# Optimization experiments

Hardware: AMD Instinct MI355X
Metric: run time of the kernel (lower is better)

The kernel has to match this reference:

```python
import jax, jax.numpy as jnp
import numpy as np
from jax import lax

EMBED = 64


def setup_inputs() -> dict:
    key = jax.random.key(0)
    ks = jax.random.split(key, 5)
    b, l, v, e, h = 256, 1024, 96, 64, 256
    x = jax.random.randint(ks[0], (b, l), 0, v, dtype=jnp.int64)
    hidden = jnp.zeros((b, h), dtype=jnp.float32)
    # xavier-uniform-like init (scale by fan sums)
    emb = jax.random.normal(ks[1], (v, e), dtype=jnp.float32) * 0.1
    W_ih = jax.random.normal(ks[2], (e + h, h), dtype=jnp.float32) * (1.0 / np.sqrt(e + h))
    b_ih = jnp.zeros((h,), dtype=jnp.float32)
    W_ho = jax.random.normal(ks[3], (h, v), dtype=jnp.float32) * (1.0 / np.sqrt(h))
    b_ho = jnp.zeros((v,), dtype=jnp.float32)
    return {"x": x, "hidden": hidden, "emb": emb, "W_ih": W_ih, "b_ih": b_ih,
            "W_ho": W_ho, "b_ho": b_ho}


def reference(x, hidden, emb, W_ih, b_ih, W_ho, b_ho):
    # x: [b, l] int indices; hidden: [b, h]
    x_embed = emb[x]                      # [b, l, e]
    Wx, Wh = W_ih[:EMBED], W_ih[EMBED:]   # split cat([x, h]) @ W_ih
    # precompute input projections for all timesteps (batched GEMM)
    xproj = jnp.einsum('ble,eh->blh', x_embed, Wx) + b_ih  # [b, l, h]

    def step(h_prev, xp_t):
        h_t = jnp.tanh(xp_t + h_prev @ Wh)  # [b, h]
        return h_t, h_t

    final_hidden, hs = lax.scan(step, hidden, xproj.transpose(1, 0, 2))  # hs: [l, b, h]
    hs = hs.transpose(1, 0, 2)                     # [b, l, h]
    logits = jnp.einsum('blh,hv->blv', hs, W_ho) + b_ho  # [b, l, v]
    return logits, final_hidden
```

## Files before the change

### kernel.cpp

```cpp
#include <hip/hip_runtime.h>
#include <hip/hip_bf16.h>

#define Lv 1024
#define Vv 96
#define Ev 64
#define Hv 256
#define ROWS 16
#define HOFF (256 * 1024 * 96)
#define EPAD 72
#define HB 4096
#define TSL 65536

typedef __attribute__((ext_vector_type(8))) short bf16x8;
typedef __attribute__((ext_vector_type(4))) float f32x4;
typedef __attribute__((ext_vector_type(2))) unsigned int u32x2;

__device__ __forceinline__ unsigned short f2b(float f) {
  unsigned u = __builtin_bit_cast(unsigned, f);
  return (unsigned short)((u + 0x7fffu + ((u >> 16) & 1u)) >> 16);
}
__device__ __forceinline__ unsigned cvtpk_bf16(float lo, float hi) {
  unsigned r;
  asm("v_cvt_pk_bf16_f32 %0, %1, %2" : "=v"(r) : "v"(lo), "v"(hi));
  return r;
}
__device__ __forceinline__ float fast_tanh(float x) {
  float e = __builtin_amdgcn_exp2f(x * 2.885390081777927f);
  return 1.0f - 2.0f * __builtin_amdgcn_rcpf(e + 1.0f);
}
__device__ __forceinline__ void step_barrier() {
  asm volatile("s_waitcnt lgkmcnt(0)\n\ts_barrier" ::: "memory");
  __builtin_amdgcn_sched_barrier(0);
}

__global__ void detect_i64(const int* __restrict__ x, int* __restrict__ flag) {
  if (threadIdx.x == 0 && blockIdx.x == 0) {
    int ok = 1;
    for (int i = 0; i < 64; ++i) ok &= (x[2 * i + 1] == 0);
    *flag = ok;
  }
}

__global__ __launch_bounds__(512, 2) void rnn8t(
    const int* __restrict__ x, const float* __restrict__ h0,
    const float* __restrict__ emb, const float* __restrict__ W_ih,
    const float* __restrict__ b_ih, float* __restrict__ out,
    unsigned short* __restrict__ hs, const int* __restrict__ flagp) {
  const int tid = threadIdx.x;
  const int w = tid >> 6, ln = tid & 63, lm = ln & 15, g = ln >> 4;
  const int r0 = blockIdx.x * ROWS;

  __shared__ __attribute__((aligned(16))) unsigned short s_h[2 * HB];
  __shared__ __attribute__((aligned(16))) unsigned short s_emb[Vv * EPAD];
  __shared__ unsigned char s_x[Lv * ROWS];

  const int flag = *flagp;

  for (int idx = tid; idx < Vv * Ev; idx += 512)
    s_emb[(idx >> 6) * EPAD + (idx & 63)] = f2b(emb[idx]);
  for (int idx = tid; idx < ROWS * Hv; idx += 512) {
    int b_ = idx >> 8, hd = idx & 255;
    s_h[HB + b_ * 256 + ((((hd >> 3) ^ (b_ & 7)) << 3) | (hd & 7))] =
        f2b(h0[(r0 + b_) * Hv + hd]);
  }
  for (int idx = tid; idx < ROWS * Lv; idx += 512) {
    int t = idx >> 4, row = idx & 15;
    long long src = (long long)(r0 + row) * Lv + t;
    int v = flag ? x[2 * src] : x[src];
    s_x[t * ROWS + row] = (unsigned char)v;
  }

  bf16x8 wh[2][8], wx[2][2];
  f32x4 bihv[2];
#pragma unroll
  for (int nt = 0; nt < 2; ++nt) {
    const int n = 32 * w + 16 * nt + lm;
#pragma unroll
    for (int kf = 0; kf < 8; ++kf)
#pragma unroll
      for (int i = 0; i < 8; ++i)
        wh[nt][kf][i] = (short)f2b(W_ih[(Ev + 32 * kf + 8 * g + i) * Hv + n]);
#pragma unroll
    for (int kf = 0; kf < 2; ++kf)
#pragma unroll
      for (int i = 0; i < 8; ++i)
        wx[nt][kf][i] = (short)f2b(W_ih[(32 * kf + 8 * g + i) * Hv + n]);
    bihv[nt] = *(const f32x4*)&b_ih[32 * w + 16 * nt + 4 * g];
  }

  const unsigned short* ra[8];
#pragma unroll
  for (int kf = 0; kf < 8; ++kf)
    ra[kf] = &s_h[lm * 256 + (((4 * kf + g) ^ (lm & 7)) << 3)];
  unsigned short* wa[2];
#pragma unroll
  for (int nt = 0; nt < 2; ++nt)
    wa[nt] = &s_h[lm * 256 + (((4 * w + 2 * nt + (g >> 1)) ^ (lm & 7)) << 3) +
                  ((g & 1) << 2)];
  unsigned short* hp = hs + (size_t)(r0 + lm) * 256 + 32 * w + 4 * g;

  __syncthreads();

  bf16x8 ef0, ef1;
  int xi_n;
  {
    int xi0 = s_x[lm];
    const unsigned short* ep = &s_emb[xi0 * EPAD + 8 * g];
    ef0 = *(const bf16x8*)ep;
    ef1 = *(const bf16x8*)(ep + 32);
    xi_n = s_x[ROWS + lm];
  }

#define STEPB(TT, RB, WB, LAST)                                                   \
  do {                                                                            \
    bf16x8 af[8];                                                                 \
    _Pragma("unroll") for (int kf = 0; kf < 8; ++kf)                              \
        af[kf] = *(const bf16x8*)(ra[kf] + (RB));                                 \
                           \
    f32x4 a0 = bihv[0];                                                           \
    a0 = __builtin_amdgcn_mfma_f32_16x16x32_bf16(wx[0][0], ef0, a0, 0, 0, 0);     \
    a0 = __builtin_amdgcn_mfma_f32_16x16x32_bf16(wx[0][1], ef1, a0, 0, 0, 0);     \
    _Pragma("unroll") for (int kf = 0; kf < 8; ++kf)                              \
        a0 = __builtin_amdgcn_mfma_f32_16x16x32_bf16(wh[0][kf], af[kf], a0, 0, 0, 0); \
    float h0v = fast_tanh(a0[0]), h1v = fast_tanh(a0[1]);                         \
    float h2v = fast_tanh(a0[2]), h3v = fast_tanh(a0[3]);                         \
    u32x2 p0;                                                                     \
    p0[0] = cvtpk_bf16(h0v, h1v);                                                 \
    p0[1] = cvtpk_bf16(h2v, h3v);                                                 \
    *(u32x2*)(wa[0] + (WB)) = p0;                  \
    *(u32x2*)hp = p0;                                           \
                                                        \
    f32x4 a1 = bihv[1];                                                           \
    a1 = __builtin_amdgcn_mfma_f32_16x16x32_bf16(wx[1][0], ef0, a1, 0, 0, 0);     \
    a1 = __builtin_amdgcn_mfma_f32_16x16x32_bf16(wx[1][1], ef1, a1, 0, 0, 0);     \
    _Pragma("unroll") for (int kf = 0; kf < 8; ++kf)                              \
        a1 = __builtin_amdgcn_mfma_f32_16x16x32_bf16(wh[1][kf], af[kf], a1, 0, 0, 0); \
    {                        \
      const unsigned short* ep = &s_emb[xi_n * EPAD + 8 * g];                     \
      ef0 = *(const bf16x8*)ep;                                                   \
      ef1 = *(const bf16x8*)(ep + 32);                                            \
      int tn = ((TT) + 2 < Lv) ? (TT) + 2 : (Lv - 1);                             \
      xi_n = s_x[tn * ROWS + lm];                                                 \
    }                                                                             \
    float h4v = fast_tanh(a1[0]), h5v = fast_tanh(a1[1]);                         \
    float h6v = fast_tanh(a1[2]), h7v = fast_tanh(a1[3]);                         \
    u32x2 p1;                                                                     \
    p1[0] = cvtpk_bf16(h4v, h5v);                                                 \
    p1[1] = cvtpk_bf16(h6v, h7v);                                                 \
    *(u32x2*)(wa[1] + (WB)) = p1;                                                 \
    *(u32x2*)(hp + 16) = p1;                                    \
    hp += TSL;                                                                    \
    if (LAST) {                                                                   \
      float* fo = out + HOFF + (size_t)(r0 + lm) * Hv + 32 * w + 4 * g;           \
      *(f32x4*)fo = (f32x4){h0v, h1v, h2v, h3v};                                  \
      *(f32x4*)(fo + 16) = (f32x4){h4v, h5v, h6v, h7v};                           \
    }                                                                             \
    step_barrier();                                                               \
  } while (0)

  STEPB(0, HB, 0, 0);
  for (int t = 1; t < Lv - 1; t += 2) {
    STEPB(t, 0, HB, 0);
    STEPB(t + 1, HB, 0, 0);
  }
  STEPB(Lv - 1, 0, HB, 1);
#undef STEPB
}

__global__ __launch_bounds__(512, 2) void logits_gemm(
    const unsigned short* __restrict__ hs, const float* __restrict__ W_ho,
    const float* __restrict__ b_ho, float* __restrict__ out) {
  const int tid = threadIdx.x;
  const int w = tid >> 6, ln = tid & 63, lm = ln & 15, g = ln >> 4;
  const int tg = blockIdx.x >> 2, bg = blockIdx.x & 3;

  __shared__ __attribute__((aligned(16))) unsigned short s_who[3072 * 8];
  for (int f = tid; f < 3072; f += 512) {
    int vt = f >> 9, kf = (f >> 6) & 7, lane = f & 63;
    int k0 = 32 * kf + 8 * (lane >> 4), v = 16 * vt + (lane & 15);
    bf16x8 fr;
#pragma unroll
    for (int i = 0; i < 8; ++i) fr[i] = (short)f2b(W_ho[(k0 + i) * Vv + v]);
    *(bf16x8*)&s_who[f * 8] = fr;
  }
  __syncthreads();

  const int bt = w & 3, vg = w >> 2;
  const int b0 = bg * 64 + bt * 16;
  const int j0 = vg * 3;
  float bb[3];
#pragma unroll
  for (int jj = 0; jj < 3; ++jj) bb[jj] = b_ho[16 * (j0 + jj) + lm];

#pragma unroll
  for (int tt = 0; tt < 4; ++tt) {
    const int t = tg * 4 + tt;
    const unsigned short* hpb = hs + (size_t)t * TSL + (b0 + lm) * 256 + 8 * g;
    f32x4 acc[3];
#pragma unroll
    for (int jj = 0; jj < 3; ++jj)
      acc[jj] = (f32x4){bb[jj], bb[jj], bb[jj], bb[jj]};
#pragma unroll
    for (int kf = 0; kf < 8; ++kf) {
      bf16x8 af = *(const bf16x8*)(hpb + 32 * kf);
#pragma unroll
      for (int jj = 0; jj < 3; ++jj) {
        bf16x8 bw = *(const bf16x8*)&s_who[(((j0 + jj) * 8 + kf) * 64 + ln) * 8];
        acc[jj] =
            __builtin_amdgcn_mfma_f32_16x16x32_bf16(af, bw, acc[jj], 0, 0, 0);
      }
    }
#pragma unroll
    for (int jj = 0; jj < 3; ++jj)
#pragma unroll
      for (int rr = 0; rr < 4; ++rr)
        out[(size_t)(b0 + 4 * g + rr) * (Lv * Vv) + (size_t)t * Vv +
            16 * (j0 + jj) + lm] = acc[jj][rr];
  }
}

__global__ __launch_bounds__(512, 2) void rnn8(
    const int* __restrict__ x, const float* __restrict__ h0,
    const float* __restrict__ emb, const float* __restrict__ W_ih,
    const float* __restrict__ b_ih, const float* __restrict__ W_ho,
    const float* __restrict__ b_ho, float* __restrict__ out,
    const int* __restrict__ flagp) {
  const int tid = threadIdx.x;
  const int w = tid >> 6, ln = tid & 63, lm = ln & 15, g = ln >> 4;
  const int r0 = blockIdx.x * ROWS;

  __shared__ __attribute__((aligned(16))) unsigned short s_emb[Vv * EPAD];
  __shared__ __attribute__((aligned(16))) unsigned short s_h[2 * HB];
  __shared__ unsigned char s_x[Lv * ROWS];

  const int flag = *flagp;

  for (int idx = tid; idx < Vv * Ev; idx += 512)
    s_emb[(idx >> 6) * EPAD + (idx & 63)] = f2b(emb[idx]);
  for (int idx = tid; idx < ROWS * Hv; idx += 512) {
    int m = idx >> 8, nn = idx & 255;
    s_h[HB + (m << 8) + ((((nn >> 3) ^ (m & 7)) << 3) | (nn & 7))] =
        f2b(h0[(r0 + m) * Hv + nn]);
  }
  for (int idx = tid; idx < ROWS * Lv; idx += 512) {
    int row = idx >> 10, t = idx & 1023;
    long long src = (long long)(r0 + row) * Lv + t;
    int v = flag ? x[2 * src] : x[src];
    s_x[t * ROWS + row] = (unsigned char)v;
  }

  bf16x8 wh[2][8], wx[2][2], who[8];
  float bih[2], bhov = 0.0f;
#pragma unroll
  for (int nt = 0; nt < 2; ++nt) {
    const int n = 32 * w + 16 * nt + lm;
    bih[nt] = b_ih[n];
#pragma unroll
    for (int kf = 0; kf < 8; ++kf)
#pragma unroll
      for (int i = 0; i < 8; ++i)
        wh[nt][kf][i] = (short)f2b(W_ih[(Ev + 32 * kf + 8 * g + i) * Hv + n]);
#pragma unroll
    for (int kf = 0; kf < 2; ++kf)
#pragma unroll
      for (int i = 0; i < 8; ++i)
        wx[nt][kf][i] = (short)f2b(W_ih[(32 * kf + 8 * g + i) * Hv + n]);
  }
  if (w < 6) {
    const int n = 16 * w + lm;
    bhov = b_ho[n];
#pragma unroll
    for (int kf = 0; kf < 8; ++kf)
#pragma unroll
      for (int i = 0; i < 8; ++i)
        who[kf][i] = (short)f2b(W_ho[(32 * kf + 8 * g + i) * Vv + n]);
  }

  const unsigned short* ra[8];
#pragma unroll
  for (int kf = 0; kf < 8; ++kf)
    ra[kf] = &s_h[(lm << 8) + (((4 * kf + g) ^ (lm & 7)) << 3)];
  unsigned short* wa[8];
#pragma unroll
  for (int nt = 0; nt < 2; ++nt)
#pragma unroll
    for (int rr = 0; rr < 4; ++rr) {
      int m = 4 * g + rr, n = 32 * w + 16 * nt + lm;
      wa[nt * 4 + rr] = &s_h[(m << 8) + ((((n >> 3) ^ (m & 7)) << 3) | (n & 7))];
    }
  float* ob[4] = {out, out, out, out};
  if (w < 6) {
#pragma unroll
    for (int rr = 0; rr < 4; ++rr)
      ob[rr] = out + (size_t)(r0 + 4 * g + rr) * (Lv * Vv) + 16 * w + lm;
  }

  __syncthreads();

  bf16x8 ef0, ef1;
  {
    int xi = s_x[lm];
    const unsigned short* ep = &s_emb[xi * EPAD + 8 * g];
    ef0 = *(const bf16x8*)ep;
    ef1 = *(const bf16x8*)(ep + 32);
  }

#define STEP8(TT, RB, WB, DOLOG, LAST)                                             \
  do {                                                                             \
    bf16x8 af[8];                                                                  \
    _Pragma("unroll") for (int kf = 0; kf < 8; ++kf)                               \
        af[kf] = *(const bf16x8*)(ra[kf] + (RB));                                  \
    f32x4 a0 = {bih[0], bih[0], bih[0], bih[0]};                                   \
    f32x4 a1 = {bih[1], bih[1], bih[1], bih[1]};                                   \
    a0 = __builtin_amdgcn_mfma_f32_16x16x32_bf16(ef0, wx[0][0], a0, 0, 0, 0);      \
    a1 = __builtin_amdgcn_mfma_f32_16x16x32_bf16(ef0, wx[1][0], a1, 0, 0, 0);      \
    a0 = __builtin_amdgcn_mfma_f32_16x16x32_bf16(ef1, wx[0][1], a0, 0, 0, 0);      \
    a1 = __builtin_amdgcn_mfma_f32_16x16x32_bf16(ef1, wx[1][1], a1, 0, 0, 0);      \
    _Pragma("unroll") for (int kf = 0; kf < 8; ++kf) {                             \
      a0 = __builtin_amdgcn_mfma_f32_16x16x32_bf16(af[kf], wh[0][kf], a0, 0, 0, 0);\
      a1 = __builtin_amdgcn_mfma_f32_16x16x32_bf16(af[kf], wh[1][kf], a1, 0, 0, 0);\
    }                                                                              \
    if ((DOLOG) && w < 6) {                                                        \
      f32x4 l = {bhov, bhov, bhov, bhov};                                          \
      _Pragma("unroll") for (int kf = 0; kf < 8; ++kf)                             \
          l = __builtin_amdgcn_mfma_f32_16x16x32_bf16(af[kf], who[kf], l, 0, 0, 0);\
      const size_t o = (size_t)((TT)-1) * Vv;                                      \
      ob[0][o] = l[0]; ob[1][o] = l[1]; ob[2][o] = l[2]; ob[3][o] = l[3];          \
    }                                                                              \
    {                                                                              \
      int tn = ((TT) + 1 < Lv) ? (TT) + 1 : (Lv - 1);                              \
      int xi = s_x[tn * ROWS + lm];                                                \
      const unsigned short* ep = &s_emb[xi * EPAD + 8 * g];                        \
      ef0 = *(const bf16x8*)ep;                                                    \
      ef1 = *(const bf16x8*)(ep + 32);                                             \
    }                                                                              \
    float th0 = fast_tanh(a0[0]), th1 = fast_tanh(a0[1]);                          \
    float th2 = fast_tanh(a0[2]), th3 = fast_tanh(a0[3]);                          \
    float th4 = fast_tanh(a1[0]), th5 = fast_tanh(a1[1]);                          \
    float th6 = fast_tanh(a1[2]), th7 = fast_tanh(a1[3]);                          \
    unsigned p01 = cvtpk_bf16(th0, th1), p23 = cvtpk_bf16(th2, th3);               \
    unsigned p45 = cvtpk_bf16(th4, th5), p67 = cvtpk_bf16(th6, th7);               \
    wa[0][WB] = (unsigned short)p01;                                               \
    wa[1][WB] = (unsigned short)(p01 >> 16);                                       \
    wa[2][WB] = (unsigned short)p23;                                               \
    wa[3][WB] = (unsigned short)(p23 >> 16);                                       \
    wa[4][WB] = (unsigned short)p45;                                               \
    wa[5][WB] = (unsigned short)(p45 >> 16);                                       \
    wa[6][WB] = (unsigned short)p67;                                               \
    wa[7][WB] = (unsigned short)(p67 >> 16);                                       \
    if (LAST) {                                                                    \
      float* fh = out + HOFF + (size_t)(r0 + 4 * g) * Hv + 32 * w + lm;            \
      fh[0 * Hv] = th0; fh[1 * Hv] = th1; fh[2 * Hv] = th2; fh[3 * Hv] = th3;      \
      fh[0 * Hv + 16] = th4; fh[1 * Hv + 16] = th5;                                \
      fh[2 * Hv + 16] = th6; fh[3 * Hv + 16] = th7;                                \
    }                                                                              \
    asm volatile("s_waitcnt lgkmcnt(0)\n\ts_barrier" ::: "memory");                \
    __builtin_amdgcn_sched_barrier(0);                                             \
  } while (0)

  STEP8(0, HB, 0, 0, 0);
  for (int t = 1; t < Lv - 1; t += 2) {
    STEP8(t, 0, HB, 1, 0);
    STEP8(t + 1, HB, 0, 1, 0);
  }
  STEP8(Lv - 1, 0, HB, 1, 1);

  if (w < 6) {
    bf16x8 af[8];
#pragma unroll
    for (int kf = 0; kf < 8; ++kf) af[kf] = *(const bf16x8*)(ra[kf] + HB);
    f32x4 l = {bhov, bhov, bhov, bhov};
#pragma unroll
    for (int kf = 0; kf < 8; ++kf)
      l = __builtin_amdgcn_mfma_f32_16x16x32_bf16(af[kf], who[kf], l, 0, 0, 0);
    const size_t o = (size_t)(Lv - 1) * Vv;
    ob[0][o] = l[0]; ob[1][o] = l[1]; ob[2][o] = l[2]; ob[3][o] = l[3];
  }
#undef STEP8
}

extern "C" void kernel_launch(void* const* d_in, const int* in_sizes, int n_in,
                              void* d_out, int out_size, void* d_ws, size_t ws_size,
                              hipStream_t stream) {
  const int* x     = (const int*)d_in[0];
  const float* h0  = (const float*)d_in[1];
  const float* emb = (const float*)d_in[2];
  const float* Wih = (const float*)d_in[3];
  const float* bih = (const float*)d_in[4];
  const float* Who = (const float*)d_in[5];
  const float* bho = (const float*)d_in[6];
  float* out = (float*)d_out;
  int* flag = (int*)d_ws;

  const size_t hs_bytes = (size_t)Lv * 256 * 256 * 2;
  detect_i64<<<1, 64, 0, stream>>>(x, flag);
  if (ws_size >= hs_bytes + 256) {
    unsigned short* hs = (unsigned short*)((char*)d_ws + 256);
    rnn8t<<<16, 512, 0, stream>>>(x, h0, emb, Wih, bih, out, hs, flag);
    logits_gemm<<<1024, 512, 0, stream>>>(hs, Who, bho, out);
  } else {
    rnn8<<<16, 512, 0, stream>>>(x, h0, emb, Wih, bih, Who, bho, out, flag);
  }
}
```

Measured before the change: 652.4 us.

## Split RNN batch across twice as many workgroups with eight rows each

The recurrent kernel now gives each workgroup 8 batch rows instead of 16 and launches 32 workgroups instead of 16, so more compute units work on the sequential recurrence at the same time. The MFMA tiles are still 16 wide, so lanes 8-15 duplicate rows 0-7 and only the lower half writes results. This shortens per-step work per CU only through more parallel blocks, not fewer MFMAs per block. Half of the MFMA work in each block is wasted, and the per-step barrier and latency chain stay the same.

```diff
diff --git a/kernel.cpp b/kernel.cpp
--- a/kernel.cpp
+++ b/kernel.cpp
@@ -6,9 +6,11 @@
 #define Ev 64
 #define Hv 256
 #define ROWS 16
+#define NBP 8
 #define HOFF (256 * 1024 * 96)
 #define EPAD 72
 #define HB 4096
+#define HBP 2048
 #define TSL 65536
 
 typedef __attribute__((ext_vector_type(8))) short bf16x8;
@@ -41,33 +43,34 @@
   }
 }
 
-__global__ __launch_bounds__(512, 2) void rnn8t(
+__global__ __launch_bounds__(512, 2) void rnn8b(
     const int* __restrict__ x, const float* __restrict__ h0,
     const float* __restrict__ emb, const float* __restrict__ W_ih,
     const float* __restrict__ b_ih, float* __restrict__ out,
     unsigned short* __restrict__ hs, const int* __restrict__ flagp) {
   const int tid = threadIdx.x;
   const int w = tid >> 6, ln = tid & 63, lm = ln & 15, g = ln >> 4;
-  const int r0 = blockIdx.x * ROWS;
-
-  __shared__ __attribute__((aligned(16))) unsigned short s_h[2 * HB];
+  const int lmb = lm & (NBP - 1);
+  const int r0 = blockIdx.x * NBP;
+
+  __shared__ __attribute__((aligned(16))) unsigned short s_h[2 * HBP];
   __shared__ __attribute__((aligned(16))) unsigned short s_emb[Vv * EPAD];
-  __shared__ unsigned char s_x[Lv * ROWS];
+  __shared__ unsigned char s_x[Lv * NBP];
 
   const int flag = *flagp;
 
   for (int idx = tid; idx < Vv * Ev; idx += 512)
     s_emb[(idx >> 6) * EPAD + (idx & 63)] = f2b(emb[idx]);
-  for (int idx = tid; idx < ROWS * Hv; idx += 512) {
+  for (int idx = tid; idx < NBP * Hv; idx += 512) {
     int b_ = idx >> 8, hd = idx & 255;
-    s_h[HB + b_ * 256 + ((((hd >> 3) ^ (b_ & 7)) << 3) | (hd & 7))] =
+    s_h[HBP + b_ * 256 + ((((hd >> 3) ^ b_) << 3) | (hd & 7))] =
         f2b(h0[(r0 + b_) * Hv + hd]);
   }
-  for (int idx = tid; idx < ROWS * Lv; idx += 512) {
-    int t = idx >> 4, row = idx & 15;
+  for (int idx = tid; idx < NBP * Lv; idx += 512) {
+    int t = idx >> 3, row = idx & (NBP - 1);
     long long src = (long long)(r0 + row) * Lv + t;
     int v = flag ? x[2 * src] : x[src];
-    s_x[t * ROWS + row] = (unsigned char)v;
+    s_x[t * NBP + row] = (unsigned char)v;
   }
 
   bf16x8 wh[2][8], wx[2][2];
@@ -91,24 +94,24 @@
   const unsigned short* ra[8];
 #pragma unroll
   for (int kf = 0; kf < 8; ++kf)
-    ra[kf] = &s_h[lm * 256 + (((4 * kf + g) ^ (lm & 7)) << 3)];
+    ra[kf] = &s_h[lmb * 256 + (((4 * kf + g) ^ lmb) << 3)];
   unsigned short* wa[2];
 #pragma unroll
   for (int nt = 0; nt < 2; ++nt)
-    wa[nt] = &s_h[lm * 256 + (((4 * w + 2 * nt + (g >> 1)) ^ (lm & 7)) << 3) +
+    wa[nt] = &s_h[lmb * 256 + (((4 * w + 2 * nt + (g >> 1)) ^ lmb) << 3) +
                   ((g & 1) << 2)];
-  unsigned short* hp = hs + (size_t)(r0 + lm) * 256 + 32 * w + 4 * g;
+  unsigned short* hp = hs + (size_t)(r0 + lmb) * 256 + 32 * w + 4 * g;
 
   __syncthreads();
 
   bf16x8 ef0, ef1;
   int xi_n;
   {
-    int xi0 = s_x[lm];
+    int xi0 = s_x[lmb];
     const unsigned short* ep = &s_emb[xi0 * EPAD + 8 * g];
     ef0 = *(const bf16x8*)ep;
     ef1 = *(const bf16x8*)(ep + 32);
-    xi_n = s_x[ROWS + lm];
+    xi_n = s_x[NBP + lmb];
   }
 
 #define STEPB(TT, RB, WB, LAST)                                                   \
@@ -127,8 +130,10 @@
     u32x2 p0;                                                                     \
     p0[0] = cvtpk_bf16(h0v, h1v);                                                 \
     p0[1] = cvtpk_bf16(h2v, h3v);                                                 \
-    *(u32x2*)(wa[0] + (WB)) = p0;                  \
-    *(u32x2*)hp = p0;                                           \
+    if (lm < NBP) {                                                               \
+      *(u32x2*)(wa[0] + (WB)) = p0;                \
+      *(u32x2*)hp = p0;                                         \
+    }                                                                             \
                                                         \
     f32x4 a1 = bihv[1];                                                           \
     a1 = __builtin_amdgcn_mfma_f32_16x16x32_bf16(wx[1][0], ef0, a1, 0, 0, 0);     \
@@ -140,30 +145,32 @@
       ef0 = *(const bf16x8*)ep;                                                   \
       ef1 = *(const bf16x8*)(ep + 32);                                            \
       int tn = ((TT) + 2 < Lv) ? (TT) + 2 : (Lv - 1);                             \
-      xi_n = s_x[tn * ROWS + lm];                                                 \
+      xi_n = s_x[tn * NBP + lmb];                                                 \
     }                                                                             \
     float h4v = fast_tanh(a1[0]), h5v = fast_tanh(a1[1]);                         \
     float h6v = fast_tanh(a1[2]), h7v = fast_tanh(a1[3]);                         \
     u32x2 p1;                                                                     \
     p1[0] = cvtpk_bf16(h4v, h5v);                                                 \
     p1[1] = cvtpk_bf16(h6v, h7v);                                                 \
-    *(u32x2*)(wa[1] + (WB)) = p1;                                                 \
-    *(u32x2*)(hp + 16) = p1;                                    \
+    if (lm < NBP) {                                                               \
+      *(u32x2*)(wa[1] + (WB)) = p1;                                               \
+      *(u32x2*)(hp + 16) = p1;                                  \
+      if (LAST) {                                                                 \
+        float* fo = out + HOFF + (size_t)(r0 + lmb) * Hv + 32 * w + 4 * g;        \
+        *(f32x4*)fo = (f32x4){h0v, h1v, h2v, h3v};                                \
+        *(f32x4*)(fo + 16) = (f32x4){h4v, h5v, h6v, h7v};                         \
+      }                                                                           \
+    }                                                                             \
     hp += TSL;                                                                    \
-    if (LAST) {                                                                   \
-      float* fo = out + HOFF + (size_t)(r0 + lm) * Hv + 32 * w + 4 * g;           \
-      *(f32x4*)fo = (f32x4){h0v, h1v, h2v, h3v};                                  \
-      *(f32x4*)(fo + 16) = (f32x4){h4v, h5v, h6v, h7v};                           \
-    }                                                                             \
     step_barrier();                                                               \
   } while (0)
 
-  STEPB(0, HB, 0, 0);
+  STEPB(0, HBP, 0, 0);
   for (int t = 1; t < Lv - 1; t += 2) {
-    STEPB(t, 0, HB, 0);
-    STEPB(t + 1, HB, 0, 0);
-  }
-  STEPB(Lv - 1, 0, HB, 1);
+    STEPB(t, 0, HBP, 0);
+    STEPB(t + 1, HBP, 0, 0);
+  }
+  STEPB(Lv - 1, 0, HBP, 1);
 #undef STEPB
 }
 
@@ -396,7 +403,7 @@
   detect_i64<<<1, 64, 0, stream>>>(x, flag);
   if (ws_size >= hs_bytes + 256) {
     unsigned short* hs = (unsigned short*)((char*)d_ws + 256);
-    rnn8t<<<16, 512, 0, stream>>>(x, h0, emb, Wih, bih, out, hs, flag);
+    rnn8b<<<32, 512, 0, stream>>>(x, h0, emb, Wih, bih, out, hs, flag);
     logits_gemm<<<1024, 512, 0, stream>>>(hs, Who, bho, out);
   } else {
     rnn8<<<16, 512, 0, stream>>>(x, h0, emb, Wih, bih, Who, bho, out, flag);
```

Measured after the change: 700.1 us. 1.07x slower.

## Use four waves per block with four interleaved MFMA chains per wave

Applied to the files above, without the earlier changes.

The recurrent kernel now runs 4 waves of 256 threads per block instead of 8 waves, and each wave computes 64 hidden columns as four 16-column tiles. The four accumulator chains are interleaved so independent MFMAs can overlap, and fewer waves share each per-step barrier. The cost is twice the register footprint for recurrent weights per thread and a longer serial MFMA sequence per wave on each timestep.

```diff
diff --git a/kernel.cpp b/kernel.cpp
--- a/kernel.cpp
+++ b/kernel.cpp
@@ -41,7 +41,7 @@
   }
 }
 
-__global__ __launch_bounds__(512, 2) void rnn8t(
+__global__ __launch_bounds__(256, 1) void rnn4w(
     const int* __restrict__ x, const float* __restrict__ h0,
     const float* __restrict__ emb, const float* __restrict__ W_ih,
     const float* __restrict__ b_ih, float* __restrict__ out,
@@ -56,25 +56,25 @@
 
   const int flag = *flagp;
 
-  for (int idx = tid; idx < Vv * Ev; idx += 512)
+  for (int idx = tid; idx < Vv * Ev; idx += 256)
     s_emb[(idx >> 6) * EPAD + (idx & 63)] = f2b(emb[idx]);
-  for (int idx = tid; idx < ROWS * Hv; idx += 512) {
+  for (int idx = tid; idx < ROWS * Hv; idx += 256) {
     int b_ = idx >> 8, hd = idx & 255;
     s_h[HB + b_ * 256 + ((((hd >> 3) ^ (b_ & 7)) << 3) | (hd & 7))] =
         f2b(h0[(r0 + b_) * Hv + hd]);
   }
-  for (int idx = tid; idx < ROWS * Lv; idx += 512) {
+  for (int idx = tid; idx < ROWS * Lv; idx += 256) {
     int t = idx >> 4, row = idx & 15;
     long long src = (long long)(r0 + row) * Lv + t;
     int v = flag ? x[2 * src] : x[src];
     s_x[t * ROWS + row] = (unsigned char)v;
   }
 
-  bf16x8 wh[2][8], wx[2][2];
-  f32x4 bihv[2];
-#pragma unroll
-  for (int nt = 0; nt < 2; ++nt) {
-    const int n = 32 * w + 16 * nt + lm;
+  bf16x8 wh[4][8], wx[4][2];
+  f32x4 bihv[4];
+#pragma unroll
+  for (int nt = 0; nt < 4; ++nt) {
+    const int n = 64 * w + 16 * nt + lm;
 #pragma unroll
     for (int kf = 0; kf < 8; ++kf)
 #pragma unroll
@@ -85,19 +85,19 @@
 #pragma unroll
       for (int i = 0; i < 8; ++i)
         wx[nt][kf][i] = (short)f2b(W_ih[(32 * kf + 8 * g + i) * Hv + n]);
-    bihv[nt] = *(const f32x4*)&b_ih[32 * w + 16 * nt + 4 * g];
+    bihv[nt] = *(const f32x4*)&b_ih[64 * w + 16 * nt + 4 * g];
   }
 
   const unsigned short* ra[8];
 #pragma unroll
   for (int kf = 0; kf < 8; ++kf)
     ra[kf] = &s_h[lm * 256 + (((4 * kf + g) ^ (lm & 7)) << 3)];
-  unsigned short* wa[2];
-#pragma unroll
-  for (int nt = 0; nt < 2; ++nt)
-    wa[nt] = &s_h[lm * 256 + (((4 * w + 2 * nt + (g >> 1)) ^ (lm & 7)) << 3) +
+  unsigned short* wa[4];
+#pragma unroll
+  for (int nt = 0; nt < 4; ++nt)
+    wa[nt] = &s_h[lm * 256 + (((8 * w + 2 * nt + (g >> 1)) ^ (lm & 7)) << 3) +
                   ((g & 1) << 2)];
-  unsigned short* hp = hs + (size_t)(r0 + lm) * 256 + 32 * w + 4 * g;
+  unsigned short* hp = hs + (size_t)(r0 + lm) * 256 + 64 * w + 4 * g;
 
   __syncthreads();
 
@@ -111,60 +111,73 @@
     xi_n = s_x[ROWS + lm];
   }
 
-#define STEPB(TT, RB, WB, LAST)                                                   \
+#define STEPW(TT, RB, WB, LAST)                                                   \
   do {                                                                            \
     bf16x8 af[8];                                                                 \
     _Pragma("unroll") for (int kf = 0; kf < 8; ++kf)                              \
         af[kf] = *(const bf16x8*)(ra[kf] + (RB));                                 \
-                           \
-    f32x4 a0 = bihv[0];                                                           \
-    a0 = __builtin_amdgcn_mfma_f32_16x16x32_bf16(wx[0][0], ef0, a0, 0, 0, 0);     \
-    a0 = __builtin_amdgcn_mfma_f32_16x16x32_bf16(wx[0][1], ef1, a0, 0, 0, 0);     \
-    _Pragma("unroll") for (int kf = 0; kf < 8; ++kf)                              \
-        a0 = __builtin_amdgcn_mfma_f32_16x16x32_bf16(wh[0][kf], af[kf], a0, 0, 0, 0); \
-    float h0v = fast_tanh(a0[0]), h1v = fast_tanh(a0[1]);                         \
-    float h2v = fast_tanh(a0[2]), h3v = fast_tanh(a0[3]);                         \
-    u32x2 p0;                                                                     \
-    p0[0] = cvtpk_bf16(h0v, h1v);                                                 \
-    p0[1] = cvtpk_bf16(h2v, h3v);                                                 \
-    *(u32x2*)(wa[0] + (WB)) = p0;                  \
-    *(u32x2*)hp = p0;                                           \
-                                                        \
-    f32x4 a1 = bihv[1];                                                           \
-    a1 = __builtin_amdgcn_mfma_f32_16x16x32_bf16(wx[1][0], ef0, a1, 0, 0, 0);     \
-    a1 = __builtin_amdgcn_mfma_f32_16x16x32_bf16(wx[1][1], ef1, a1, 0, 0, 0);     \
-    _Pragma("unroll") for (int kf = 0; kf < 8; ++kf)                              \
-        a1 = __builtin_amdgcn_mfma_f32_16x16x32_bf16(wh[1][kf], af[kf], a1, 0, 0, 0); \
-    {                        \
+               \
+    f32x4 c0 = bihv[0], c1 = bihv[1], c2 = bihv[2], c3 = bihv[3];                 \
+    c0 = __builtin_amdgcn_mfma_f32_16x16x32_bf16(wx[0][0], ef0, c0, 0, 0, 0);     \
+    c1 = __builtin_amdgcn_mfma_f32_16x16x32_bf16(wx[1][0], ef0, c1, 0, 0, 0);     \
+    c2 = __builtin_amdgcn_mfma_f32_16x16x32_bf16(wx[2][0], ef0, c2, 0, 0, 0);     \
+    c3 = __builtin_amdgcn_mfma_f32_16x16x32_bf16(wx[3][0], ef0, c3, 0, 0, 0);     \
+    c0 = __builtin_amdgcn_mfma_f32_16x16x32_bf16(wx[0][1], ef1, c0, 0, 0, 0);     \
+    c1 = __builtin_amdgcn_mfma_f32_16x16x32_bf16(wx[1][1], ef1, c1, 0, 0, 0);     \
+    c2 = __builtin_amdgcn_mfma_f32_16x16x32_bf16(wx[2][1], ef1, c2, 0, 0, 0);     \
+    c3 = __builtin_amdgcn_mfma_f32_16x16x32_bf16(wx[3][1], ef1, c3, 0, 0, 0);     \
+    _Pragma("unroll") for (int kf = 0; kf < 8; ++kf) {                            \
+      c0 = __builtin_amdgcn_mfma_f32_16x16x32_bf16(wh[0][kf], af[kf], c0, 0, 0, 0); \
+      c1 = __builtin_amdgcn_mfma_f32_16x16x32_bf16(wh[1][kf], af[kf], c1, 0, 0, 0); \
+      c2 = __builtin_amdgcn_mfma_f32_16x16x32_bf16(wh[2][kf], af[kf], c2, 0, 0, 0); \
+      c3 = __builtin_amdgcn_mfma_f32_16x16x32_bf16(wh[3][kf], af[kf], c3, 0, 0, 0); \
+    }                                                                             \
+    {                            \
       const unsigned short* ep = &s_emb[xi_n * EPAD + 8 * g];                     \
       ef0 = *(const bf16x8*)ep;                                                   \
       ef1 = *(const bf16x8*)(ep + 32);                                            \
       int tn = ((TT) + 2 < Lv) ? (TT) + 2 : (Lv - 1);                             \
       xi_n = s_x[tn * ROWS + lm];                                                 \
     }                                                                             \
-    float h4v = fast_tanh(a1[0]), h5v = fast_tanh(a1[1]);                         \
-    float h6v = fast_tanh(a1[2]), h7v = fast_tanh(a1[3]);                         \
-    u32x2 p1;                                                                     \
-    p1[0] = cvtpk_bf16(h4v, h5v);                                                 \
-    p1[1] = cvtpk_bf16(h6v, h7v);                                                 \
+    float t0 = fast_tanh(c0[0]), t1 = fast_tanh(c0[1]);                           \
+    float t2 = fast_tanh(c0[2]), t3 = fast_tanh(c0[3]);                           \
+    float t4 = fast_tanh(c1[0]), t5 = fast_tanh(c1[1]);                           \
+    float t6 = fast_tanh(c1[2]), t7 = fast_tanh(c1[3]);                           \
+    float t8 = fast_tanh(c2[0]), t9 = fast_tanh(c2[1]);                           \
+    float ta = fast_tanh(c2[2]), tb = fast_tanh(c2[3]);                           \
+    float tc = fast_tanh(c3[0]), td = fast_tanh(c3[1]);                           \
+    float te = fast_tanh(c3[2]), tf = fast_tanh(c3[3]);                           \
+    u32x2 p0, p1, p2, p3;                                                         \
+    p0[0] = cvtpk_bf16(t0, t1); p0[1] = cvtpk_bf16(t2, t3);                       \
+    p1[0] = cvtpk_bf16(t4, t5); p1[1] = cvtpk_bf16(t6, t7);                       \
+    p2[0] = cvtpk_bf16(t8, t9); p2[1] = cvtpk_bf16(ta, tb);                       \
+    p3[0] = cvtpk_bf16(tc, td); p3[1] = cvtpk_bf16(te, tf);                       \
+    *(u32x2*)(wa[0] + (WB)) = p0;                                                 \
     *(u32x2*)(wa[1] + (WB)) = p1;                                                 \
-    *(u32x2*)(hp + 16) = p1;                                    \
+    *(u32x2*)(wa[2] + (WB)) = p2;                                                 \
+    *(u32x2*)(wa[3] + (WB)) = p3;                                                 \
+    *(u32x2*)hp = p0;                                           \
+    *(u32x2*)(hp + 16) = p1;                                            \
+    *(u32x2*)(hp + 32) = p2;                                            \
+    *(u32x2*)(hp + 48) = p3;                                            \
     hp += TSL;                                                                    \
     if (LAST) {                                                                   \
-      float* fo = out + HOFF + (size_t)(r0 + lm) * Hv + 32 * w + 4 * g;           \
-      *(f32x4*)fo = (f32x4){h0v, h1v, h2v, h3v};                                  \
-      *(f32x4*)(fo + 16) = (f32x4){h4v, h5v, h6v, h7v};                           \
+      float* fo = out + HOFF + (size_t)(r0 + lm) * Hv + 64 * w + 4 * g;           \
+      *(f32x4*)fo = (f32x4){t0, t1, t2, t3};                                      \
+      *(f32x4*)(fo + 16) = (f32x4){t4, t5, t6, t7};                               \
+      *(f32x4*)(fo + 32) = (f32x4){t8, t9, ta, tb};                               \
+      *(f32x4*)(fo + 48) = (f32x4){tc, td, te, tf};                               \
     }                                                                             \
     step_barrier();                                                               \
   } while (0)
 
-  STEPB(0, HB, 0, 0);
+  STEPW(0, HB, 0, 0);
   for (int t = 1; t < Lv - 1; t += 2) {
-    STEPB(t, 0, HB, 0);
-    STEPB(t + 1, HB, 0, 0);
-  }
-  STEPB(Lv - 1, 0, HB, 1);
-#undef STEPB
+    STEPW(t, 0, HB, 0);
+    STEPW(t + 1, HB, 0, 0);
+  }
+  STEPW(Lv - 1, 0, HB, 1);
+#undef STEPW
 }
 
 __global__ __launch_bounds__(512, 2) void logits_gemm(
@@ -396,7 +409,7 @@
   detect_i64<<<1, 64, 0, stream>>>(x, flag);
   if (ws_size >= hs_bytes + 256) {
     unsigned short* hs = (unsigned short*)((char*)d_ws + 256);
-    rnn8t<<<16, 512, 0, stream>>>(x, h0, emb, Wih, bih, out, hs, flag);
+    rnn4w<<<16, 256, 0, stream>>>(x, h0, emb, Wih, bih, out, hs, flag);
     logits_gemm<<<1024, 512, 0, stream>>>(hs, Who, bho, out);
   } else {
     rnn8<<<16, 512, 0, stream>>>(x, h0, emb, Wih, bih, Who, bho, out, flag);
```

After: 778.7 us. 1.19x slower.
